# Performance work log

Measured on AMD Instinct MI355X. Metric: run time of the kernel, lower is better.

The kernel has to match this reference:

```python
import jax, jax.numpy as jnp
import numpy as np

D_MODEL = 1024
N_HEADS = 16
D_HEAD = D_MODEL // N_HEADS


def setup_inputs() -> dict:
    key = jax.random.key(0)
    ks = jax.random.split(key, 11)
    s = 0.02
    return {
        "X": jax.random.normal(ks[0], (4, 2048, D_MODEL), dtype=jnp.float32),
        "ln_gamma": jnp.ones((D_MODEL,), jnp.float32),
        "ln_beta": jnp.zeros((D_MODEL,), jnp.float32),
        "Wq": jax.random.normal(ks[1], (D_MODEL, D_MODEL), jnp.float32) * s,
        "bq": jnp.zeros((D_MODEL,), jnp.float32),
        "Wk": jax.random.normal(ks[2], (D_MODEL, D_MODEL), jnp.float32) * s,
        "bk": jnp.zeros((D_MODEL,), jnp.float32),
        "Wv": jax.random.normal(ks[3], (D_MODEL, D_MODEL), jnp.float32) * s,
        "bv": jnp.zeros((D_MODEL,), jnp.float32),
        "Wo": jax.random.normal(ks[4], (D_MODEL, D_MODEL), jnp.float32) * s,
        "bo": jnp.zeros((D_MODEL,), jnp.float32),
    }


def _attention(X, ln_gamma, ln_beta, Wq, bq, Wk, bk, Wv, bv, Wo, bo):
    B, S, D = X.shape
    H, Dh = N_HEADS, D_HEAD
    # LayerNorm over last dim
    mu = jnp.mean(X, axis=-1, keepdims=True)
    var = jnp.mean(jnp.square(X - mu), axis=-1, keepdims=True)
    Xn = (X - mu) * jax.lax.rsqrt(var + 1e-5) * ln_gamma + ln_beta
    # Projections (torch Linear: x @ W.T + b; W is [out, in])
    Q = (Xn @ Wq.T + bq).reshape(B, S, H, Dh).transpose(0, 2, 1, 3)
    K = (Xn @ Wk.T + bk).reshape(B, S, H, Dh).transpose(0, 2, 1, 3)
    V = (Xn @ Wv.T + bv).reshape(B, S, H, Dh).transpose(0, 2, 1, 3)
    scale = 1.0 / np.sqrt(Dh).astype(np.float32)
    scores = jnp.einsum("bhqd,bhkd->bhqk", Q * scale, K)  # [B,H,S,S]
    # p_dropout = 0.0 -> dropout is identity (applied before mask in original)
    # additive causal mask: 0 where q >= k, -inf otherwise
    causal = jnp.tril(jnp.ones((S, S), jnp.bool_))
    scores = jnp.where(causal, scores, -jnp.inf)
    A = jax.nn.softmax(scores, axis=-1)
    AV = jnp.einsum("bhqk,bhkd->bhqd", A, V)
    merged = AV.transpose(0, 2, 1, 3).reshape(B, S, D)
    return merged @ Wo.T + bo


def reference(X, ln_gamma, ln_beta, Wq, bq, Wk, bk, Wv, bv, Wo, bo):
    return _attention(X, ln_gamma, ln_beta, Wq, bq, Wk, bk, Wv, bv, Wo, bo)
```

## Files before the change

kernel.cpp:

```cpp
#include <hip/hip_runtime.h>

#define D_MODEL 1024
#define N_HEADS 16
#define D_HEAD 64
#define BATCH 4
#define SEQ 2048
#define TOKENS (BATCH * SEQ)

#define QBLK 64
#define KBLK 64

typedef __attribute__((ext_vector_type(8))) short short8;
typedef __attribute__((ext_vector_type(4))) float f32x4;

__device__ __forceinline__ unsigned short f2bf(float f) {
    unsigned u = __float_as_uint(f);
    u += 0x7fffu + ((u >> 16) & 1u);
    return (unsigned short)(u >> 16);
}
__device__ __forceinline__ float bf2f(unsigned short s) {
    return __uint_as_float(((unsigned)s) << 16);
}
__device__ __forceinline__ void gload16(const unsigned short* g, unsigned short* lds) {
    __builtin_amdgcn_global_load_lds((const __attribute__((address_space(1))) void*)g,
                                     (__attribute__((address_space(3))) void*)lds, 16, 0, 0);
}

__global__ void ln_kernel(const float* __restrict__ X, const float* __restrict__ gamma,
                          const float* __restrict__ beta, unsigned short* __restrict__ Xn) {
    const int t = blockIdx.x;
    const int tid = threadIdx.x;
    const float4 v = ((const float4*)(X + (size_t)t * D_MODEL))[tid];
    float s  = v.x + v.y + v.z + v.w;
    float s2 = v.x * v.x + v.y * v.y + v.z * v.z + v.w * v.w;
    for (int off = 32; off > 0; off >>= 1) {
        s  += __shfl_xor(s,  off);
        s2 += __shfl_xor(s2, off);
    }
    __shared__ float sh[8];
    const int wv = tid >> 6;
    if ((tid & 63) == 0) { sh[wv] = s; sh[4 + wv] = s2; }
    __syncthreads();
    const float ts  = sh[0] + sh[1] + sh[2] + sh[3];
    const float ts2 = sh[4] + sh[5] + sh[6] + sh[7];
    const float mu  = ts * (1.0f / D_MODEL);
    const float var = ts2 * (1.0f / D_MODEL) - mu * mu;
    const float rs  = rsqrtf(var + 1e-5f);
    const float4 gm = ((const float4*)gamma)[tid];
    const float4 bt = ((const float4*)beta)[tid];
    ushort4 o;
    o.x = f2bf((v.x - mu) * rs * gm.x + bt.x);
    o.y = f2bf((v.y - mu) * rs * gm.y + bt.y);
    o.z = f2bf((v.z - mu) * rs * gm.z + bt.z);
    o.w = f2bf((v.w - mu) * rs * gm.w + bt.w);
    ((ushort4*)Xn)[(size_t)t * (D_MODEL / 4) + tid] = o;
}

__global__ void cvt_kernel(const float* __restrict__ src, unsigned short* __restrict__ dst) {
    const int i = blockIdx.x * blockDim.x + threadIdx.x;
    const float4 v = ((const float4*)src)[i];
    ushort4 o;
    o.x = f2bf(v.x); o.y = f2bf(v.y); o.z = f2bf(v.z); o.w = f2bf(v.w);
    ((ushort4*)dst)[i] = o;
}

__global__ void transpose_v(const unsigned short* __restrict__ in, unsigned short* __restrict__ out) {
    __shared__ __attribute__((aligned(16))) unsigned short T[64][72];
    const int tid = threadIdx.x;
    const int s0 = blockIdx.x * 64;
    const int n0 = blockIdx.y * 64;
    const int b  = blockIdx.z;
    const int r = tid >> 2, c = (tid & 3) * 16;
    const unsigned short* ip = in + ((size_t)(b * SEQ + s0 + r)) * D_MODEL + n0 + c;
    *(short8*)&T[r][c]     = *(const short8*)ip;
    *(short8*)&T[r][c + 8] = *(const short8*)(ip + 8);
    __syncthreads();
    unsigned short* op = out + ((size_t)(b * D_MODEL + n0 + r)) * SEQ + s0 + c;
    short8 o0, o1;
    #pragma unroll
    for (int j = 0; j < 8; ++j) { o0[j] = (short)T[c + j][r]; o1[j] = (short)T[c + 8 + j][r]; }
    *(short8*)op       = o0;
    *(short8*)(op + 8) = o1;
}

template <bool OUT_BF16>
__global__ __launch_bounds__(256) void gemm128(const unsigned short* __restrict__ A,
                                               const unsigned short* __restrict__ B,
                                               const float* __restrict__ bias, void* __restrict__ out,
                                               int M, int N, int K, float oscale) {
    __shared__ __attribute__((aligned(16))) unsigned short As[128 * 64];
    __shared__ __attribute__((aligned(16))) unsigned short Bs[128 * 64];
    const int tid  = threadIdx.x;
    const int lane = tid & 63;
    const int w    = tid >> 6;
    const int wm = w >> 1, wn = w & 1;
    const int m0 = blockIdx.y * 128;
    const int n0 = blockIdx.x * 128;
    const int lr = lane & 15, lg = lane >> 4;

    const int crow  = lane >> 3;
    const int uslot = (lane & 7) ^ crow;

    f32x4 acc[4][4] = {};
    for (int k0 = 0; k0 < K; k0 += 64) {
        __syncthreads();
        #pragma unroll
        for (int i = 0; i < 4; ++i) {
            const int c = w * 4 + i;
            const int grow = c * 8 + crow;
            gload16(A + (size_t)(m0 + grow) * K + k0 + uslot * 8, As + c * 512);
            gload16(B + (size_t)(n0 + grow) * K + k0 + uslot * 8, Bs + c * 512);
        }
        __syncthreads();
        #pragma unroll
        for (int h = 0; h < 2; ++h) {
            short8 af[4], bf[4];
            #pragma unroll
            for (int mi = 0; mi < 4; ++mi) {
                const int row = wm * 64 + mi * 16 + lr;
                const int slot = (h * 4 + lg) ^ (row & 7);
                af[mi] = *(const short8*)(As + row * 64 + slot * 8);
            }
            #pragma unroll
            for (int ni = 0; ni < 4; ++ni) {
                const int row = wn * 64 + ni * 16 + lr;
                const int slot = (h * 4 + lg) ^ (row & 7);
                bf[ni] = *(const short8*)(Bs + row * 64 + slot * 8);
            }
            #pragma unroll
            for (int mi = 0; mi < 4; ++mi)
                #pragma unroll
                for (int ni = 0; ni < 4; ++ni)
                    acc[mi][ni] = __builtin_amdgcn_mfma_f32_16x16x32_bf16(af[mi], bf[ni], acc[mi][ni], 0, 0, 0);
        }
    }
    #pragma unroll
    for (int ni = 0; ni < 4; ++ni) {
        const int n = n0 + wn * 64 + ni * 16 + lr;
        const float bv = bias[n];
        #pragma unroll
        for (int mi = 0; mi < 4; ++mi) {
            const int mb = m0 + wm * 64 + mi * 16 + lg * 4;
            #pragma unroll
            for (int i = 0; i < 4; ++i) {
                const float val = (acc[mi][ni][i] + bv) * oscale;
                if (OUT_BF16) ((unsigned short*)out)[(size_t)(mb + i) * N + n] = f2bf(val);
                else          ((float*)out)[(size_t)(mb + i) * N + n] = val;
            }
        }
    }
}

__global__ __launch_bounds__(256) void flash_attn(const unsigned short* __restrict__ Q,
                                                  const unsigned short* __restrict__ K,
                                                  const unsigned short* __restrict__ Vt,
                                                  unsigned short* __restrict__ Mo) {
    __shared__ __attribute__((aligned(16))) unsigned short KtL[2][KBLK * 64];
    __shared__ __attribute__((aligned(16))) unsigned short VsL[2][64 * KBLK];
    __shared__ __attribute__((aligned(16))) unsigned short Pq[4 * 4 * 16 * 16];

    const int tid  = threadIdx.x;
    const int lane = tid & 63;
    const int w    = tid >> 6;
    const int F   = blockIdx.x;
    const int xcd = F & 7;
    const int r_  = F >> 3;
    const int qb  = 31 - (r_ & 31);
    const int bh  = xcd | ((r_ >> 5) << 3);
    const int b = bh >> 4, h = bh & 15;
    const int q0 = qb * QBLK;
    const int lg = lane >> 4;
    const int lr = lane & 15;

    const size_t tokbase = (size_t)b * SEQ;
    const size_t hoff = (size_t)h * D_HEAD;

    const int crow  = lane >> 3;
    const int uslot = (lane & 7) ^ crow;

    const short* Qp = (const short*)Q + (tokbase + q0 + w * 16 + lr) * D_MODEL + hoff + lg * 8;
    const short8 qf0 = *(const short8*)(Qp);
    const short8 qf1 = *(const short8*)(Qp + 32);

    int koff[2][4];
    #pragma unroll
    for (int hh = 0; hh < 2; ++hh)
        #pragma unroll
        for (int s4 = 0; s4 < 4; ++s4)
            koff[hh][s4] = (s4 * 16 + lr) * 64 + (((hh * 4 + lg) ^ (lr & 7)) * 8);
    const int pwbase = (w * 4) * 256 + (lg * 4) * 16 + lr;
    int prd[2];
    #pragma unroll
    for (int c2 = 0; c2 < 2; ++c2)
        prd[c2] = (w * 4 + c2 * 2 + (lg >> 1)) * 256 + lr * 16 + (lg & 1) * 8;

    float m[4], l[4];
    f32x4 acc[4];
    #pragma unroll
    for (int i = 0; i < 4; ++i) { m[i] = -INFINITY; l[i] = 0.f; acc[i] = (f32x4){0.f,0.f,0.f,0.f}; }

    const int ntiles = qb + 1;

    {
        #pragma unroll
        for (int i = 0; i < 2; ++i) {
            const int c = w * 2 + i;
            const int row = c * 8 + crow;
            gload16(K + (tokbase + row) * D_MODEL + hoff + uslot * 8, &KtL[0][c * 512]);
            gload16(Vt + ((size_t)bh * 64 + row) * SEQ + uslot * 8, &VsL[0][c * 512]);
        }
    }
    __syncthreads();

    int cur = 0;
    for (int t = 0; t < ntiles; ++t) {
        if (t + 1 < ntiles) {
            const int k1 = (t + 1) * KBLK;
            #pragma unroll
            for (int i = 0; i < 2; ++i) {
                const int c = w * 2 + i;
                const int row = c * 8 + crow;
                gload16(K + (tokbase + k1 + row) * D_MODEL + hoff + uslot * 8, &KtL[cur ^ 1][c * 512]);
                gload16(Vt + ((size_t)bh * 64 + row) * SEQ + k1 + uslot * 8, &VsL[cur ^ 1][c * 512]);
            }
        }
        const unsigned short* Kc = KtL[cur];
        const unsigned short* Vc = VsL[cur];

        f32x4 sc[4];
        #pragma unroll
        for (int s4 = 0; s4 < 4; ++s4) {
            const short8 kf0 = *(const short8*)(Kc + koff[0][s4]);
            const short8 kf1 = *(const short8*)(Kc + koff[1][s4]);
            f32x4 z = {0.f, 0.f, 0.f, 0.f};
            z = __builtin_amdgcn_mfma_f32_16x16x32_bf16(qf0, kf0, z, 0, 0, 0);
            z = __builtin_amdgcn_mfma_f32_16x16x32_bf16(qf1, kf1, z, 0, 0, 0);
            sc[s4] = z;
        }

        if (t == qb) {
            const int qr = w * 16 + lg * 4;
            #pragma unroll
            for (int s4 = 0; s4 < 4; ++s4) {
                const int kk = s4 * 16 + lr;
                #pragma unroll
                for (int i = 0; i < 4; ++i)
                    sc[s4][i] = (kk <= qr + i) ? sc[s4][i] : -INFINITY;
            }
        }

        float c_[4];
        #pragma unroll
        for (int i = 0; i < 4; ++i) {
            float rm = fmaxf(fmaxf(sc[0][i], sc[1][i]), fmaxf(sc[2][i], sc[3][i]));
            rm = fmaxf(rm, __shfl_xor(rm, 1));
            rm = fmaxf(rm, __shfl_xor(rm, 2));
            rm = fmaxf(rm, __shfl_xor(rm, 4));
            rm = fmaxf(rm, __shfl_xor(rm, 8));
            const float mn = fmaxf(m[i], rm);
            c_[i] = __builtin_exp2f(m[i] - mn);
            m[i] = mn;
        }
        #pragma unroll
        for (int i = 0; i < 4; ++i) {
            float rs = 0.f;
            #pragma unroll
            for (int s4 = 0; s4 < 4; ++s4) {
                const float p = __builtin_exp2f(sc[s4][i] - m[i]);
                sc[s4][i] = p;
                rs += p;
            }
            rs += __shfl_xor(rs, 1); rs += __shfl_xor(rs, 2);
            rs += __shfl_xor(rs, 4); rs += __shfl_xor(rs, 8);
            l[i] = l[i] * c_[i] + rs;
            #pragma unroll
            for (int ds = 0; ds < 4; ++ds) acc[ds][i] *= c_[i];
        }

        #pragma unroll
        for (int s4 = 0; s4 < 4; ++s4)
            #pragma unroll
            for (int i = 0; i < 4; ++i) {
                const unsigned u = __float_as_uint(sc[s4][i]) + 0x8000u;
                Pq[pwbase + s4 * 256 + i * 16] = (unsigned short)(u >> 16);
            }

        #pragma unroll
        for (int c2 = 0; c2 < 2; ++c2) {
            const short8 pf = *(const short8*)(Pq + prd[c2]);
            #pragma unroll
            for (int ds = 0; ds < 4; ++ds) {
                const short8 vf = *(const short8*)(Vc + koff[c2][ds]);
                acc[ds] = __builtin_amdgcn_mfma_f32_16x16x32_bf16(pf, vf, acc[ds], 0, 0, 0);
            }
        }

        __syncthreads();
        cur ^= 1;
    }

    const int gq = q0 + w * 16 + lg * 4;
    #pragma unroll
    for (int ds = 0; ds < 4; ++ds) {
        const float inv = 1.0f;
        #pragma unroll
        for (int i = 0; i < 4; ++i) {
            const float o = acc[ds][i] / l[i];
            Mo[(tokbase + gq + i) * D_MODEL + hoff + ds * 16 + lr] = f2bf(o);
        }
        (void)inv;
    }
}

extern "C" void kernel_launch(void* const* d_in, const int* in_sizes, int n_in,
                              void* d_out, int out_size, void* d_ws, size_t ws_size,
                              hipStream_t stream) {
    const float* X  = (const float*)d_in[0];
    const float* lg = (const float*)d_in[1];
    const float* lb = (const float*)d_in[2];
    const float* Wq = (const float*)d_in[3];
    const float* bq = (const float*)d_in[4];
    const float* Wk = (const float*)d_in[5];
    const float* bk = (const float*)d_in[6];
    const float* Wv = (const float*)d_in[7];
    const float* bv = (const float*)d_in[8];
    const float* Wo = (const float*)d_in[9];
    const float* bo = (const float*)d_in[10];
    float* out = (float*)d_out;

    char* ws = (char*)d_ws;
    const size_t MB = 1024 * 1024;
    unsigned short* Xn  = (unsigned short*)(ws + 0);
    unsigned short* WqB = (unsigned short*)(ws + 16 * MB);
    unsigned short* WkB = (unsigned short*)(ws + 18 * MB);
    unsigned short* WvB = (unsigned short*)(ws + 20 * MB);
    unsigned short* WoB = (unsigned short*)(ws + 22 * MB);
    unsigned short* Qb  = (unsigned short*)(ws + 24 * MB);
    unsigned short* Kb  = (unsigned short*)(ws + 40 * MB);
    unsigned short* Vb  = (unsigned short*)(ws + 56 * MB);
    unsigned short* Vtg = (unsigned short*)(ws + 72 * MB);
    unsigned short* Mb  = (unsigned short*)(ws + 56 * MB);

    ln_kernel<<<TOKENS, 256, 0, stream>>>(X, lg, lb, Xn);

    cvt_kernel<<<1024, 256, 0, stream>>>(Wq, WqB);
    cvt_kernel<<<1024, 256, 0, stream>>>(Wk, WkB);
    cvt_kernel<<<1024, 256, 0, stream>>>(Wv, WvB);
    cvt_kernel<<<1024, 256, 0, stream>>>(Wo, WoB);

    dim3 ggrid(D_MODEL / 128, TOKENS / 128);
    const float qscale = 0.125f * 1.44269504088896f;
    gemm128<true><<<ggrid, 256, 0, stream>>>(Xn, WqB, bq, Qb, TOKENS, D_MODEL, D_MODEL, qscale);
    gemm128<true><<<ggrid, 256, 0, stream>>>(Xn, WkB, bk, Kb, TOKENS, D_MODEL, D_MODEL, 1.0f);
    gemm128<true><<<ggrid, 256, 0, stream>>>(Xn, WvB, bv, Vb, TOKENS, D_MODEL, D_MODEL, 1.0f);

    dim3 tgrid(SEQ / 64, D_MODEL / 64, BATCH);
    transpose_v<<<tgrid, 256, 0, stream>>>(Vb, Vtg);

    flash_attn<<<(SEQ / QBLK) * BATCH * N_HEADS, 256, 0, stream>>>(Qb, Kb, Vtg, Mb);

    gemm128<false><<<ggrid, 256, 0, stream>>>(Mb, WoB, bo, out, TOKENS, D_MODEL, D_MODEL, 1.0f);
}
```

Before: 373.6 us.

## Fuse QKV projections, double-buffer GEMM, lazy softmax rescale, pad P buffer

Merges the three projection GEMMs into one GEMM over a concatenated QKV weight, and merges the four weight conversion launches into one. The GEMM now double-buffers its LDS tiles so global loads overlap compute. In flash attention, the running-max rescale is skipped unless the max grows by more than a threshold, the P staging buffer is padded to reduce LDS bank conflicts, and MFMA sections get raised wave priority. The aim is fewer launches, less load latency, and less softmax work, at the cost of more LDS in the GEMM, which may lower occupancy.

```diff
diff --git a/kernel.cpp b/kernel.cpp
--- a/kernel.cpp
+++ b/kernel.cpp
@@ -6,6 +6,7 @@
 #define BATCH 4
 #define SEQ 2048
 #define TOKENS (BATCH * SEQ)
+#define D_QKV 3072
 
 #define QBLK 64
 #define KBLK 64
@@ -17,9 +18,6 @@
     unsigned u = __float_as_uint(f);
     u += 0x7fffu + ((u >> 16) & 1u);
     return (unsigned short)(u >> 16);
-}
-__device__ __forceinline__ float bf2f(unsigned short s) {
-    return __uint_as_float(((unsigned)s) << 16);
 }
 __device__ __forceinline__ void gload16(const unsigned short* g, unsigned short* lds) {
     __builtin_amdgcn_global_load_lds((const __attribute__((address_space(1))) void*)g,
@@ -56,22 +54,32 @@
     ((ushort4*)Xn)[(size_t)t * (D_MODEL / 4) + tid] = o;
 }
 
-__global__ void cvt_kernel(const float* __restrict__ src, unsigned short* __restrict__ dst) {
+__global__ void cvt_all(const float* __restrict__ Wq, const float* __restrict__ Wk,
+                        const float* __restrict__ Wv, const float* __restrict__ Wo,
+                        unsigned short* __restrict__ Wqkv, unsigned short* __restrict__ WoB) {
     const int i = blockIdx.x * blockDim.x + threadIdx.x;
-    const float4 v = ((const float4*)src)[i];
+    const int mtx  = i >> 18;
+    const int elem = i & 262143;
+    const float* src;
+    unsigned short* dst;
+    if (mtx == 0)      { src = Wq; dst = Wqkv; }
+    else if (mtx == 1) { src = Wk; dst = Wqkv + (1 << 20); }
+    else if (mtx == 2) { src = Wv; dst = Wqkv + (2 << 20); }
+    else               { src = Wo; dst = WoB; }
+    const float4 v = ((const float4*)src)[elem];
     ushort4 o;
     o.x = f2bf(v.x); o.y = f2bf(v.y); o.z = f2bf(v.z); o.w = f2bf(v.w);
-    ((ushort4*)dst)[i] = o;
-}
-
-__global__ void transpose_v(const unsigned short* __restrict__ in, unsigned short* __restrict__ out) {
+    ((ushort4*)dst)[elem] = o;
+}
+
+__global__ void transpose_v(const unsigned short* __restrict__ QKV, unsigned short* __restrict__ out) {
     __shared__ __attribute__((aligned(16))) unsigned short T[64][72];
     const int tid = threadIdx.x;
     const int s0 = blockIdx.x * 64;
     const int n0 = blockIdx.y * 64;
     const int b  = blockIdx.z;
     const int r = tid >> 2, c = (tid & 3) * 16;
-    const unsigned short* ip = in + ((size_t)(b * SEQ + s0 + r)) * D_MODEL + n0 + c;
+    const unsigned short* ip = QKV + ((size_t)(b * SEQ + s0 + r)) * D_QKV + 2048 + n0 + c;
     *(short8*)&T[r][c]     = *(const short8*)ip;
     *(short8*)&T[r][c + 8] = *(const short8*)(ip + 8);
     __syncthreads();
@@ -86,10 +94,13 @@
 template <bool OUT_BF16>
 __global__ __launch_bounds__(256) void gemm128(const unsigned short* __restrict__ A,
                                                const unsigned short* __restrict__ B,
-                                               const float* __restrict__ bias, void* __restrict__ out,
-                                               int M, int N, int K, float oscale) {
-    __shared__ __attribute__((aligned(16))) unsigned short As[128 * 64];
-    __shared__ __attribute__((aligned(16))) unsigned short Bs[128 * 64];
+                                               const float* __restrict__ b0,
+                                               const float* __restrict__ b1,
+                                               const float* __restrict__ b2,
+                                               void* __restrict__ out,
+                                               int M, int N, int K, float qscale) {
+    __shared__ __attribute__((aligned(16))) unsigned short As[2][128 * 64];
+    __shared__ __attribute__((aligned(16))) unsigned short Bs[2][128 * 64];
     const int tid  = threadIdx.x;
     const int lane = tid & 63;
     const int w    = tid >> 6;
@@ -101,17 +112,32 @@
     const int crow  = lane >> 3;
     const int uslot = (lane & 7) ^ crow;
 
+    const unsigned short* Ab = A + (size_t)m0 * K + uslot * 8;
+    const unsigned short* Bb = B + (size_t)n0 * K + uslot * 8;
+
+    #pragma unroll
+    for (int i = 0; i < 4; ++i) {
+        const int c = w * 4 + i;
+        const int grow = c * 8 + crow;
+        gload16(Ab + (size_t)grow * K, &As[0][c * 512]);
+        gload16(Bb + (size_t)grow * K, &Bs[0][c * 512]);
+    }
+    __syncthreads();
+
     f32x4 acc[4][4] = {};
-    for (int k0 = 0; k0 < K; k0 += 64) {
-        __syncthreads();
-        #pragma unroll
-        for (int i = 0; i < 4; ++i) {
-            const int c = w * 4 + i;
-            const int grow = c * 8 + crow;
-            gload16(A + (size_t)(m0 + grow) * K + k0 + uslot * 8, As + c * 512);
-            gload16(B + (size_t)(n0 + grow) * K + k0 + uslot * 8, Bs + c * 512);
-        }
-        __syncthreads();
+    const int NT = K >> 6;
+    int cur = 0;
+    for (int kt = 0; kt < NT; ++kt) {
+        if (kt + 1 < NT) {
+            const int k1 = (kt + 1) << 6;
+            #pragma unroll
+            for (int i = 0; i < 4; ++i) {
+                const int c = w * 4 + i;
+                const int grow = c * 8 + crow;
+                gload16(Ab + (size_t)grow * K + k1, &As[cur ^ 1][c * 512]);
+                gload16(Bb + (size_t)grow * K + k1, &Bs[cur ^ 1][c * 512]);
+            }
+        }
         #pragma unroll
         for (int h = 0; h < 2; ++h) {
             short8 af[4], bf[4];
@@ -119,13 +145,13 @@
             for (int mi = 0; mi < 4; ++mi) {
                 const int row = wm * 64 + mi * 16 + lr;
                 const int slot = (h * 4 + lg) ^ (row & 7);
-                af[mi] = *(const short8*)(As + row * 64 + slot * 8);
+                af[mi] = *(const short8*)(&As[cur][row * 64 + slot * 8]);
             }
             #pragma unroll
             for (int ni = 0; ni < 4; ++ni) {
                 const int row = wn * 64 + ni * 16 + lr;
                 const int slot = (h * 4 + lg) ^ (row & 7);
-                bf[ni] = *(const short8*)(Bs + row * 64 + slot * 8);
+                bf[ni] = *(const short8*)(&Bs[cur][row * 64 + slot * 8]);
             }
             #pragma unroll
             for (int mi = 0; mi < 4; ++mi)
@@ -133,17 +159,23 @@
                 for (int ni = 0; ni < 4; ++ni)
                     acc[mi][ni] = __builtin_amdgcn_mfma_f32_16x16x32_bf16(af[mi], bf[ni], acc[mi][ni], 0, 0, 0);
         }
-    }
+        __syncthreads();
+        cur ^= 1;
+    }
+
+    const int seg = blockIdx.x >> 3;
+    const float* bp = (seg == 0) ? b0 : (seg == 1) ? b1 : b2;
+    const float osc = (seg == 0) ? qscale : 1.0f;
     #pragma unroll
     for (int ni = 0; ni < 4; ++ni) {
         const int n = n0 + wn * 64 + ni * 16 + lr;
-        const float bv = bias[n];
+        const float bv = bp[n & 1023];
         #pragma unroll
         for (int mi = 0; mi < 4; ++mi) {
             const int mb = m0 + wm * 64 + mi * 16 + lg * 4;
             #pragma unroll
             for (int i = 0; i < 4; ++i) {
-                const float val = (acc[mi][ni][i] + bv) * oscale;
+                const float val = (acc[mi][ni][i] + bv) * osc;
                 if (OUT_BF16) ((unsigned short*)out)[(size_t)(mb + i) * N + n] = f2bf(val);
                 else          ((float*)out)[(size_t)(mb + i) * N + n] = val;
             }
@@ -151,13 +183,12 @@
     }
 }
 
-__global__ __launch_bounds__(256) void flash_attn(const unsigned short* __restrict__ Q,
-                                                  const unsigned short* __restrict__ K,
+__global__ __launch_bounds__(256) void flash_attn(const unsigned short* __restrict__ QKV,
                                                   const unsigned short* __restrict__ Vt,
                                                   unsigned short* __restrict__ Mo) {
     __shared__ __attribute__((aligned(16))) unsigned short KtL[2][KBLK * 64];
     __shared__ __attribute__((aligned(16))) unsigned short VsL[2][64 * KBLK];
-    __shared__ __attribute__((aligned(16))) unsigned short Pq[4 * 4 * 16 * 16];
+    __shared__ __attribute__((aligned(16))) unsigned short Pq[4 * 4 * 16 * 24];
 
     const int tid  = threadIdx.x;
     const int lane = tid & 63;
@@ -178,21 +209,24 @@
     const int crow  = lane >> 3;
     const int uslot = (lane & 7) ^ crow;
 
-    const short* Qp = (const short*)Q + (tokbase + q0 + w * 16 + lr) * D_MODEL + hoff + lg * 8;
+    const short* Qp = (const short*)QKV + (tokbase + q0 + w * 16 + lr) * D_QKV + hoff + lg * 8;
     const short8 qf0 = *(const short8*)(Qp);
     const short8 qf1 = *(const short8*)(Qp + 32);
 
+    const unsigned short* Kg = QKV + (tokbase) * D_QKV + 1024 + hoff + uslot * 8;
+    const unsigned short* Vg = Vt + ((size_t)bh * 64) * SEQ + uslot * 8;
+
     int koff[2][4];
     #pragma unroll
     for (int hh = 0; hh < 2; ++hh)
         #pragma unroll
         for (int s4 = 0; s4 < 4; ++s4)
             koff[hh][s4] = (s4 * 16 + lr) * 64 + (((hh * 4 + lg) ^ (lr & 7)) * 8);
-    const int pwbase = (w * 4) * 256 + (lg * 4) * 16 + lr;
+    const int pwbase = w * 1536 + lg * 96 + lr;
     int prd[2];
     #pragma unroll
     for (int c2 = 0; c2 < 2; ++c2)
-        prd[c2] = (w * 4 + c2 * 2 + (lg >> 1)) * 256 + lr * 16 + (lg & 1) * 8;
+        prd[c2] = w * 1536 + (c2 * 2 + (lg >> 1)) * 384 + lr * 24 + (lg & 1) * 8;
 
     float m[4], l[4];
     f32x4 acc[4];
@@ -201,14 +235,12 @@
 
     const int ntiles = qb + 1;
 
-    {
-        #pragma unroll
-        for (int i = 0; i < 2; ++i) {
-            const int c = w * 2 + i;
-            const int row = c * 8 + crow;
-            gload16(K + (tokbase + row) * D_MODEL + hoff + uslot * 8, &KtL[0][c * 512]);
-            gload16(Vt + ((size_t)bh * 64 + row) * SEQ + uslot * 8, &VsL[0][c * 512]);
-        }
+    #pragma unroll
+    for (int i = 0; i < 2; ++i) {
+        const int c = w * 2 + i;
+        const int row = c * 8 + crow;
+        gload16(Kg + (size_t)row * D_QKV, &KtL[0][c * 512]);
+        gload16(Vg + (size_t)row * SEQ, &VsL[0][c * 512]);
     }
     __syncthreads();
 
@@ -220,14 +252,15 @@
             for (int i = 0; i < 2; ++i) {
                 const int c = w * 2 + i;
                 const int row = c * 8 + crow;
-                gload16(K + (tokbase + k1 + row) * D_MODEL + hoff + uslot * 8, &KtL[cur ^ 1][c * 512]);
-                gload16(Vt + ((size_t)bh * 64 + row) * SEQ + k1 + uslot * 8, &VsL[cur ^ 1][c * 512]);
+                gload16(Kg + (size_t)(k1 + row) * D_QKV, &KtL[cur ^ 1][c * 512]);
+                gload16(Vg + (size_t)row * SEQ + k1, &VsL[cur ^ 1][c * 512]);
             }
         }
         const unsigned short* Kc = KtL[cur];
         const unsigned short* Vc = VsL[cur];
 
         f32x4 sc[4];
+        __builtin_amdgcn_s_setprio(1);
         #pragma unroll
         for (int s4 = 0; s4 < 4; ++s4) {
             const short8 kf0 = *(const short8*)(Kc + koff[0][s4]);
@@ -237,6 +270,7 @@
             z = __builtin_amdgcn_mfma_f32_16x16x32_bf16(qf1, kf1, z, 0, 0, 0);
             sc[s4] = z;
         }
+        __builtin_amdgcn_s_setprio(0);
 
         if (t == qb) {
             const int qr = w * 16 + lg * 4;
@@ -249,18 +283,30 @@
             }
         }
 
-        float c_[4];
+        float rm[4];
+        bool need = false;
         #pragma unroll
         for (int i = 0; i < 4; ++i) {
-            float rm = fmaxf(fmaxf(sc[0][i], sc[1][i]), fmaxf(sc[2][i], sc[3][i]));
-            rm = fmaxf(rm, __shfl_xor(rm, 1));
-            rm = fmaxf(rm, __shfl_xor(rm, 2));
-            rm = fmaxf(rm, __shfl_xor(rm, 4));
-            rm = fmaxf(rm, __shfl_xor(rm, 8));
-            const float mn = fmaxf(m[i], rm);
-            c_[i] = __builtin_exp2f(m[i] - mn);
-            m[i] = mn;
-        }
+            float r = fmaxf(fmaxf(sc[0][i], sc[1][i]), fmaxf(sc[2][i], sc[3][i]));
+            r = fmaxf(r, __shfl_xor(r, 1));
+            r = fmaxf(r, __shfl_xor(r, 2));
+            r = fmaxf(r, __shfl_xor(r, 4));
+            r = fmaxf(r, __shfl_xor(r, 8));
+            rm[i] = r;
+            need |= (r > m[i] + 8.0f);
+        }
+        if (__any(need)) {
+            #pragma unroll
+            for (int i = 0; i < 4; ++i) {
+                const float mn = fmaxf(m[i], rm[i]);
+                const float c  = __builtin_exp2f(m[i] - mn);
+                m[i] = mn;
+                l[i] *= c;
+                #pragma unroll
+                for (int ds = 0; ds < 4; ++ds) acc[ds][i] *= c;
+            }
+        }
+
         #pragma unroll
         for (int i = 0; i < 4; ++i) {
             float rs = 0.f;
@@ -272,19 +318,17 @@
             }
             rs += __shfl_xor(rs, 1); rs += __shfl_xor(rs, 2);
             rs += __shfl_xor(rs, 4); rs += __shfl_xor(rs, 8);
-            l[i] = l[i] * c_[i] + rs;
-            #pragma unroll
-            for (int ds = 0; ds < 4; ++ds) acc[ds][i] *= c_[i];
-        }
-
+            l[i] += rs;
+        }
         #pragma unroll
         for (int s4 = 0; s4 < 4; ++s4)
             #pragma unroll
             for (int i = 0; i < 4; ++i) {
                 const unsigned u = __float_as_uint(sc[s4][i]) + 0x8000u;
-                Pq[pwbase + s4 * 256 + i * 16] = (unsigned short)(u >> 16);
-            }
-
+                Pq[pwbase + s4 * 384 + i * 24] = (unsigned short)(u >> 16);
+            }
+
+        __builtin_amdgcn_s_setprio(1);
         #pragma unroll
         for (int c2 = 0; c2 < 2; ++c2) {
             const short8 pf = *(const short8*)(Pq + prd[c2]);
@@ -294,6 +338,7 @@
                 acc[ds] = __builtin_amdgcn_mfma_f32_16x16x32_bf16(pf, vf, acc[ds], 0, 0, 0);
             }
         }
+        __builtin_amdgcn_s_setprio(0);
 
         __syncthreads();
         cur ^= 1;
@@ -302,13 +347,11 @@
     const int gq = q0 + w * 16 + lg * 4;
     #pragma unroll
     for (int ds = 0; ds < 4; ++ds) {
-        const float inv = 1.0f;
         #pragma unroll
         for (int i = 0; i < 4; ++i) {
             const float o = acc[ds][i] / l[i];
             Mo[(tokbase + gq + i) * D_MODEL + hoff + ds * 16 + lr] = f2bf(o);
         }
-        (void)inv;
     }
 }
 
@@ -330,34 +373,28 @@
 
     char* ws = (char*)d_ws;
     const size_t MB = 1024 * 1024;
-    unsigned short* Xn  = (unsigned short*)(ws + 0);
-    unsigned short* WqB = (unsigned short*)(ws + 16 * MB);
-    unsigned short* WkB = (unsigned short*)(ws + 18 * MB);
-    unsigned short* WvB = (unsigned short*)(ws + 20 * MB);
-    unsigned short* WoB = (unsigned short*)(ws + 22 * MB);
-    unsigned short* Qb  = (unsigned short*)(ws + 24 * MB);
-    unsigned short* Kb  = (unsigned short*)(ws + 40 * MB);
-    unsigned short* Vb  = (unsigned short*)(ws + 56 * MB);
-    unsigned short* Vtg = (unsigned short*)(ws + 72 * MB);
-    unsigned short* Mb  = (unsigned short*)(ws + 56 * MB);
+    unsigned short* Xn   = (unsigned short*)(ws + 0);
+    unsigned short* Vtg  = (unsigned short*)(ws + 0);
+    unsigned short* Wqkv = (unsigned short*)(ws + 16 * MB);
+    unsigned short* WoB  = (unsigned short*)(ws + 22 * MB);
+    unsigned short* QKVb = (unsigned short*)(ws + 24 * MB);
+    unsigned short* Mb   = (unsigned short*)(ws + 72 * MB);
 
     ln_kernel<<<TOKENS, 256, 0, stream>>>(X, lg, lb, Xn);
 
-    cvt_kernel<<<1024, 256, 0, stream>>>(Wq, WqB);
-    cvt_kernel<<<1024, 256, 0, stream>>>(Wk, WkB);
-    cvt_kernel<<<1024, 256, 0, stream>>>(Wv, WvB);
-    cvt_kernel<<<1024, 256, 0, stream>>>(Wo, WoB);
-
-    dim3 ggrid(D_MODEL / 128, TOKENS / 128);
+    cvt_all<<<4096, 256, 0, stream>>>(Wq, Wk, Wv, Wo, Wqkv, WoB);
+
     const float qscale = 0.125f * 1.44269504088896f;
-    gemm128<true><<<ggrid, 256, 0, stream>>>(Xn, WqB, bq, Qb, TOKENS, D_MODEL, D_MODEL, qscale);
-    gemm128<true><<<ggrid, 256, 0, stream>>>(Xn, WkB, bk, Kb, TOKENS, D_MODEL, D_MODEL, 1.0f);
-    gemm128<true><<<ggrid, 256, 0, stream>>>(Xn, WvB, bv, Vb, TOKENS, D_MODEL, D_MODEL, 1.0f);
+    dim3 qkvgrid(D_QKV / 128, TOKENS / 128);
+    gemm128<true><<<qkvgrid, 256, 0, stream>>>(Xn, Wqkv, bq, bk, bv, QKVb,
+                                               TOKENS, D_QKV, D_MODEL, qscale);
 
     dim3 tgrid(SEQ / 64, D_MODEL / 64, BATCH);
-    transpose_v<<<tgrid, 256, 0, stream>>>(Vb, Vtg);
-
-    flash_attn<<<(SEQ / QBLK) * BATCH * N_HEADS, 256, 0, stream>>>(Qb, Kb, Vtg, Mb);
-
-    gemm128<false><<<ggrid, 256, 0, stream>>>(Mb, WoB, bo, out, TOKENS, D_MODEL, D_MODEL, 1.0f);
-}
+    transpose_v<<<tgrid, 256, 0, stream>>>(QKVb, Vtg);
+
+    flash_attn<<<(SEQ / QBLK) * BATCH * N_HEADS, 256, 0, stream>>>(QKVb, Vtg, Mb);
+
+    dim3 ogrid(D_MODEL / 128, TOKENS / 128);
+    gemm128<false><<<ogrid, 256, 0, stream>>>(Mb, WoB, bo, bo, bo, out,
+                                              TOKENS, D_MODEL, D_MODEL, 1.0f);
+}
```

Measured after the change: 359.2 us. -3.9%, faster.
